# Kernel optimization log

Measured on AMD Instinct MI355X. Metric: run time of the kernel, lower is better.

The kernel has to match this reference:

```python
import jax, jax.numpy as jnp
import numpy as np


def setup_inputs() -> dict:
    key = jax.random.key(0)
    ks = jax.random.split(key, 5)
    B, T, D, H = 32, 2048, 512, 512
    return {
        "x": jax.random.normal(ks[0], (B, T, D), dtype=jnp.float32),
        "W_w": jax.random.normal(ks[1], (4 * H, D), dtype=jnp.float32) * 0.05,
        "W_b": jax.random.normal(ks[2], (4 * H,), dtype=jnp.float32) * 0.05,
        "U_w": jax.random.normal(ks[3], (4 * H, H), dtype=jnp.float32) * 0.05,
        "U_b": jax.random.normal(ks[4], (4 * H,), dtype=jnp.float32) * 0.05,
        "alpha": jnp.ones((H,), dtype=jnp.float32),
    }


def reference(x, W_w, W_b, U_w, U_b, alpha):
    B, T, D = x.shape
    H = alpha.shape[0]
    # Precompute input projection for all timesteps: [B, T, 4H]
    wx = jnp.einsum("btd,gd->btg", x, W_w) + W_b
    h0 = jnp.zeros((B, H), dtype=x.dtype)
    c0 = jnp.zeros((B, H), dtype=x.dtype)

    def step(carry, wx_t):
        h, c = carry
        gates = wx_t + h @ U_w.T + U_b  # [B, 4H]
        i, f, o, g = jnp.split(gates, 4, axis=-1)
        i = jax.nn.sigmoid(i)
        f = jax.nn.sigmoid(f)
        o = jax.nn.sigmoid(o)
        g = jnp.tanh(g)
        c = alpha * (f * c + i * g)
        h = o * jnp.tanh(c)
        return (h, c), h

    (h, c), outs = jax.lax.scan(step, (h0, c0), jnp.swapaxes(wx, 0, 1))
    outs = jnp.swapaxes(outs, 0, 1)  # [B, T, H]
    return outs, (h, c)
```

## Files before the change

kernel.cpp:

```cpp
#include <hip/hip_runtime.h>

#define TT 2048
#define BB 32
#define HH 512
#define NWG 32

typedef _Float16 half8 __attribute__((ext_vector_type(8)));
typedef float f32x4 __attribute__((ext_vector_type(4)));

__device__ __forceinline__ float fsig(float x) { return 1.f / (1.f + __expf(-x)); }
__device__ __forceinline__ float ftanh_(float x) {
  x = fminf(fmaxf(x, -15.f), 15.f);
  float e = __expf(2.f * x);
  return (e - 1.f) / (e + 1.f);
}

__global__ void cvt_f32_f16(const float* __restrict__ in, _Float16* __restrict__ out, int n4) {
  int i = blockIdx.x * 256 + threadIdx.x;
  if (i >= n4) return;
  float4 v = ((const float4*)in)[i];
  union { _Float16 h[4]; unsigned long long u; } r;
  r.h[0] = (_Float16)v.x; r.h[1] = (_Float16)v.y;
  r.h[2] = (_Float16)v.z; r.h[3] = (_Float16)v.w;
  ((unsigned long long*)out)[i] = r.u;
}

__global__ __launch_bounds__(256, 2) void gemm_wx(const _Float16* __restrict__ A,
                                                  const _Float16* __restrict__ Bw,
                                                  _Float16* __restrict__ C) {
  const int bn = blockIdx.x;
  const int bm = blockIdx.y;
  const int tid = threadIdx.x;
  const int lane = tid & 63;
  const int w = tid >> 6;
  __shared__ _Float16 As[128 * 40];
  __shared__ _Float16 Bs[128 * 40];
  const int moff = (w & 1) * 64;
  const int noff = (w >> 1) * 64;
  const int fm = lane & 15;
  const int kq = lane >> 4;
  f32x4 acc[4][4] = {};
  for (int kt = 0; kt < 16; ++kt) {
#pragma unroll
    for (int e = 0; e < 2; ++e) {
      int ci = tid * 2 + e;
      int r = ci >> 2, c16 = ci & 3;
      half8 av = *(const half8*)(A + (size_t)(bm * 128 + r) * 512 + kt * 32 + c16 * 8);
      half8 bv = *(const half8*)(Bw + (size_t)(bn * 128 + r) * 512 + kt * 32 + c16 * 8);
      *(half8*)(As + r * 40 + c16 * 8) = av;
      *(half8*)(Bs + r * 40 + c16 * 8) = bv;
    }
    __syncthreads();
    half8 af[4], bf[4];
#pragma unroll
    for (int i = 0; i < 4; ++i) {
      af[i] = *(const half8*)(As + (moff + i * 16 + fm) * 40 + kq * 8);
      bf[i] = *(const half8*)(Bs + (noff + i * 16 + fm) * 40 + kq * 8);
    }
#pragma unroll
    for (int i = 0; i < 4; ++i)
#pragma unroll
      for (int j = 0; j < 4; ++j)
        acc[i][j] = __builtin_amdgcn_mfma_f32_16x16x32_f16(af[i], bf[j], acc[i][j], 0, 0, 0);
    __syncthreads();
  }
#pragma unroll
  for (int i = 0; i < 4; ++i) {
    int row = bm * 128 + moff + i * 16 + (lane >> 4) * 4;
#pragma unroll
    for (int j = 0; j < 4; ++j) {
      int col = bn * 128 + noff + j * 16 + (lane & 15);
#pragma unroll
      for (int r = 0; r < 4; ++r)
        C[(size_t)(row + r) * 2048 + col] = (_Float16)acc[i][j][r];
    }
  }
}

__global__ __launch_bounds__(256, 1) void slstm_scan(
    const _Float16* __restrict__ wx,
    const _Float16* __restrict__ U16,
    const float* __restrict__ Wb, const float* __restrict__ Ub,
    const float* __restrict__ alpha,
    _Float16* __restrict__ hex,
    int* __restrict__ flags,
    float* __restrict__ out) {
  const int g = blockIdx.x;
  const int tid = threadIdx.x;
  const int lane = tid & 63;
  const int w = tid >> 6;
  const int mi = w & 1;
  const int qA = (w >> 1) * 2;
  const int ncol = lane & 15;
  const int kq = lane >> 4;
  const int am = mi * 16 + ncol;

  half8 Bf0[16], Bf1[16];
#pragma unroll
  for (int ks = 0; ks < 16; ++ks) {
    Bf0[ks] = *(const half8*)(U16 + (size_t)(qA * 512 + g * 16 + ncol) * 512 + ks * 32 + kq * 8);
    Bf1[ks] = *(const half8*)(U16 + (size_t)((qA + 1) * 512 + g * 16 + ncol) * 512 + ks * 32 + kq * 8);
  }

  const int eb = tid >> 3;
  const int jp = tid & 7;
  const int gj0 = g * 16 + jp * 2;
  float bias0[4], bias1[4];
#pragma unroll
  for (int q = 0; q < 4; ++q) {
    bias0[q] = Wb[q * 512 + gj0] + Ub[q * 512 + gj0];
    bias1[q] = Wb[q * 512 + gj0 + 1] + Ub[q * 512 + gj0 + 1];
  }
  const float al0 = alpha[gj0], al1 = alpha[gj0 + 1];
  float c0 = 0.f, c1 = 0.f;

  __shared__ float Sg[4 * 32 * 18];
  __shared__ _Float16 Swx[4 * 32 * 16];

  const int lq = tid >> 6;
  const int lb = (tid >> 1) & 31;
  const int lc = tid & 1;
  const _Float16* wxp = wx + (size_t)lb * TT * 2048 + lq * 512 + g * 16 + lc * 8;

  int spin_budget = 1 << 23;
  const int fl = lane & 31;

  for (int t = 0; t < TT; ++t) {
    half8 wxv = *(const half8*)(wxp + (size_t)t * 2048);
    f32x4 acc0 = {0.f, 0.f, 0.f, 0.f}, acc1 = {0.f, 0.f, 0.f, 0.f};
    if (t > 0) {
      int* fp = flags + (size_t)(t - 1) * 32;
      int v;
      do {
        v = __hip_atomic_load(fp + fl, __ATOMIC_RELAXED, __HIP_MEMORY_SCOPE_AGENT);
        if (--spin_budget <= 0) break;
      } while (!__all(v != 0));
      asm volatile("" ::: "memory");
      unsigned long long* hb64 =
          (unsigned long long*)(hex + ((t & 1) ^ 1) * (BB * HH) + (size_t)am * HH);
      union { unsigned long long u[2]; half8 h; } af[16];
#pragma unroll
      for (int ks = 0; ks < 16; ++ks) {
        af[ks].u[0] = __hip_atomic_load(hb64 + ks * 8 + kq * 2,
                                        __ATOMIC_RELAXED, __HIP_MEMORY_SCOPE_AGENT);
        af[ks].u[1] = __hip_atomic_load(hb64 + ks * 8 + kq * 2 + 1,
                                        __ATOMIC_RELAXED, __HIP_MEMORY_SCOPE_AGENT);
      }
#pragma unroll
      for (int ks = 0; ks < 16; ++ks) {
        acc0 = __builtin_amdgcn_mfma_f32_16x16x32_f16(af[ks].h, Bf0[ks], acc0, 0, 0, 0);
        acc1 = __builtin_amdgcn_mfma_f32_16x16x32_f16(af[ks].h, Bf1[ks], acc1, 0, 0, 0);
      }
    }
    *(half8*)(Swx + (lq * 32 + lb) * 16 + lc * 8) = wxv;
#pragma unroll
    for (int i = 0; i < 4; ++i) {
      int m = mi * 16 + kq * 4 + i;
      Sg[(qA * 32 + m) * 18 + ncol] = acc0[i];
      Sg[((qA + 1) * 32 + m) * 18 + ncol] = acc1[i];
    }
    __syncthreads();
    float p0[4], p1[4];
#pragma unroll
    for (int q = 0; q < 4; ++q) {
      const int so = (q * 32 + eb) * 18 + jp * 2;
      const int wo = (q * 32 + eb) * 16 + jp * 2;
      p0[q] = Sg[so] + (float)Swx[wo] + bias0[q];
      p1[q] = Sg[so + 1] + (float)Swx[wo + 1] + bias1[q];
    }
    float i0 = fsig(p0[0]), f0 = fsig(p0[1]), o0 = fsig(p0[2]), g0 = ftanh_(p0[3]);
    float i1 = fsig(p1[0]), f1 = fsig(p1[1]), o1 = fsig(p1[2]), g1 = ftanh_(p1[3]);
    c0 = al0 * (f0 * c0 + i0 * g0);
    c1 = al1 * (f1 * c1 + i1 * g1);
    float h0 = o0 * ftanh_(c0);
    float h1 = o1 * ftanh_(c1);
    union { _Float16 h[2]; unsigned int u; } pk;
    pk.h[0] = (_Float16)h0; pk.h[1] = (_Float16)h1;
    unsigned int* hx = (unsigned int*)hex + ((t & 1) * (BB * HH) + eb * HH + gj0) / 2;
    __hip_atomic_store(hx, pk.u, __ATOMIC_RELAXED, __HIP_MEMORY_SCOPE_AGENT);
    asm volatile("s_waitcnt vmcnt(0)" ::: "memory");
    __syncthreads();
    if (tid == 0)
      __hip_atomic_store(flags + (size_t)t * 32 + g, 1,
                         __ATOMIC_RELAXED, __HIP_MEMORY_SCOPE_AGENT);
    size_t ob = ((size_t)eb * TT + t) * HH + gj0;
    union { float f[2]; double d; } od;
    od.f[0] = h0; od.f[1] = h1;
    __builtin_nontemporal_store(od.d, (double*)(out + ob));
    if (t == TT - 1) {
      const size_t HB = (size_t)BB * TT * HH;
      out[HB + eb * HH + gj0] = h0;
      out[HB + eb * HH + gj0 + 1] = h1;
      out[HB + BB * HH + eb * HH + gj0] = c0;
      out[HB + BB * HH + eb * HH + gj0 + 1] = c1;
    }
  }
}

extern "C" void kernel_launch(void* const* d_in, const int* in_sizes, int n_in,
                              void* d_out, int out_size, void* d_ws, size_t ws_size,
                              hipStream_t stream) {
  (void)in_sizes; (void)n_in; (void)out_size; (void)ws_size;
  const float* x  = (const float*)d_in[0];
  const float* Ww = (const float*)d_in[1];
  const float* Wb = (const float*)d_in[2];
  const float* Uw = (const float*)d_in[3];
  const float* Ub = (const float*)d_in[4];
  const float* al = (const float*)d_in[5];
  float* out = (float*)d_out;

  char* p = (char*)d_ws;
  _Float16* x16  = (_Float16*)p; p += (size_t)BB * TT * 512 * 2;
  _Float16* wx16 = (_Float16*)p; p += (size_t)BB * TT * 2048 * 2;
  _Float16* U16  = (_Float16*)p; p += (size_t)2048 * 512 * 2;
  _Float16* W16  = (_Float16*)p; p += (size_t)2048 * 512 * 2;
  _Float16* hexb = (_Float16*)p; p += (size_t)2 * BB * HH * 2;
  int* flags     = (int*)p;      p += (size_t)TT * 32 * 4;

  (void)hipMemsetAsync(flags, 0, (size_t)TT * 32 * 4, stream);
  cvt_f32_f16<<<32768, 256, 0, stream>>>(x, x16, BB * TT * 512 / 4);
  cvt_f32_f16<<<1024, 256, 0, stream>>>(Ww, W16, 2048 * 512 / 4);
  cvt_f32_f16<<<1024, 256, 0, stream>>>(Uw, U16, 2048 * 512 / 4);
  gemm_wx<<<dim3(16, 512), 256, 0, stream>>>(x16, W16, wx16);
  slstm_scan<<<NWG, 256, 0, stream>>>(wx16, U16, Wb, Ub, al, hexb, flags, out);
}
```

Baseline: 12.21 ms.

## Replace flag-based inter-block sync with sentinel-filled per-timestep hidden-state buffer

Drops the per-timestep flag array and the write, wait, barrier and flag-store handshake. Each timestep now writes h into its own slice of a buffer pre-filled with 0xFF (a NaN sentinel, reusing the x16 workspace after the GEMM), and consumers spin directly on the h data until no sentinel values remain. This removes one round trip of global-memory latency per step on the serial critical path. In exchange it costs a large memset and relies on no valid fp16 h pair matching the sentinel pattern, and it only checks that each 32-bit word was written, not the ordering of separate stores.

```diff
diff --git a/kernel.cpp b/kernel.cpp
--- a/kernel.cpp
+++ b/kernel.cpp
@@ -83,7 +83,6 @@
     const float* __restrict__ Wb, const float* __restrict__ Ub,
     const float* __restrict__ alpha,
     _Float16* __restrict__ hex,
-    int* __restrict__ flags,
     float* __restrict__ out) {
   const int g = blockIdx.x;
   const int tid = threadIdx.x;
@@ -122,29 +121,33 @@
   const int lc = tid & 1;
   const _Float16* wxp = wx + (size_t)lb * TT * 2048 + lq * 512 + g * 16 + lc * 8;
 
-  int spin_budget = 1 << 23;
-  const int fl = lane & 31;
+  int spin_budget = 1 << 22;
 
   for (int t = 0; t < TT; ++t) {
     half8 wxv = *(const half8*)(wxp + (size_t)t * 2048);
     f32x4 acc0 = {0.f, 0.f, 0.f, 0.f}, acc1 = {0.f, 0.f, 0.f, 0.f};
     if (t > 0) {
-      int* fp = flags + (size_t)(t - 1) * 32;
-      int v;
-      do {
-        v = __hip_atomic_load(fp + fl, __ATOMIC_RELAXED, __HIP_MEMORY_SCOPE_AGENT);
+      const unsigned long long* hb64 =
+          (const unsigned long long*)(hex + (size_t)(t - 1) * (BB * HH) + (size_t)am * HH);
+      union { unsigned long long u[2]; half8 h; } af[16];
+      for (;;) {
+        unsigned mx = 0;
+#pragma unroll
+        for (int ks = 0; ks < 16; ++ks) {
+          af[ks].u[0] = __hip_atomic_load(hb64 + ks * 8 + kq * 2,
+                                          __ATOMIC_RELAXED, __HIP_MEMORY_SCOPE_AGENT);
+          af[ks].u[1] = __hip_atomic_load(hb64 + ks * 8 + kq * 2 + 1,
+                                          __ATOMIC_RELAXED, __HIP_MEMORY_SCOPE_AGENT);
+        }
+#pragma unroll
+        for (int ks = 0; ks < 16; ++ks) {
+          unsigned a = (unsigned)af[ks].u[0], b = (unsigned)(af[ks].u[0] >> 32);
+          unsigned c = (unsigned)af[ks].u[1], d = (unsigned)(af[ks].u[1] >> 32);
+          mx = mx > a ? mx : a; mx = mx > b ? mx : b;
+          mx = mx > c ? mx : c; mx = mx > d ? mx : d;
+        }
+        if (__all(mx < 0xFFFF0000u)) break;
         if (--spin_budget <= 0) break;
-      } while (!__all(v != 0));
-      asm volatile("" ::: "memory");
-      unsigned long long* hb64 =
-          (unsigned long long*)(hex + ((t & 1) ^ 1) * (BB * HH) + (size_t)am * HH);
-      union { unsigned long long u[2]; half8 h; } af[16];
-#pragma unroll
-      for (int ks = 0; ks < 16; ++ks) {
-        af[ks].u[0] = __hip_atomic_load(hb64 + ks * 8 + kq * 2,
-                                        __ATOMIC_RELAXED, __HIP_MEMORY_SCOPE_AGENT);
-        af[ks].u[1] = __hip_atomic_load(hb64 + ks * 8 + kq * 2 + 1,
-                                        __ATOMIC_RELAXED, __HIP_MEMORY_SCOPE_AGENT);
       }
 #pragma unroll
       for (int ks = 0; ks < 16; ++ks) {
@@ -176,13 +179,8 @@
     float h1 = o1 * ftanh_(c1);
     union { _Float16 h[2]; unsigned int u; } pk;
     pk.h[0] = (_Float16)h0; pk.h[1] = (_Float16)h1;
-    unsigned int* hx = (unsigned int*)hex + ((t & 1) * (BB * HH) + eb * HH + gj0) / 2;
+    unsigned int* hx = (unsigned int*)hex + ((size_t)t * (BB * HH) + eb * HH + gj0) / 2;
     __hip_atomic_store(hx, pk.u, __ATOMIC_RELAXED, __HIP_MEMORY_SCOPE_AGENT);
-    asm volatile("s_waitcnt vmcnt(0)" ::: "memory");
-    __syncthreads();
-    if (tid == 0)
-      __hip_atomic_store(flags + (size_t)t * 32 + g, 1,
-                         __ATOMIC_RELAXED, __HIP_MEMORY_SCOPE_AGENT);
     size_t ob = ((size_t)eb * TT + t) * HH + gj0;
     union { float f[2]; double d; } od;
     od.f[0] = h0; od.f[1] = h1;
@@ -194,6 +192,7 @@
       out[HB + BB * HH + eb * HH + gj0] = c0;
       out[HB + BB * HH + eb * HH + gj0 + 1] = c1;
     }
+    __syncthreads();
   }
 }
 
@@ -214,13 +213,12 @@
   _Float16* wx16 = (_Float16*)p; p += (size_t)BB * TT * 2048 * 2;
   _Float16* U16  = (_Float16*)p; p += (size_t)2048 * 512 * 2;
   _Float16* W16  = (_Float16*)p; p += (size_t)2048 * 512 * 2;
-  _Float16* hexb = (_Float16*)p; p += (size_t)2 * BB * HH * 2;
-  int* flags     = (int*)p;      p += (size_t)TT * 32 * 4;
-
-  (void)hipMemsetAsync(flags, 0, (size_t)TT * 32 * 4, stream);
+  _Float16* hexb = x16;
+
   cvt_f32_f16<<<32768, 256, 0, stream>>>(x, x16, BB * TT * 512 / 4);
   cvt_f32_f16<<<1024, 256, 0, stream>>>(Ww, W16, 2048 * 512 / 4);
   cvt_f32_f16<<<1024, 256, 0, stream>>>(Uw, U16, 2048 * 512 / 4);
   gemm_wx<<<dim3(16, 512), 256, 0, stream>>>(x16, W16, wx16);
-  slstm_scan<<<NWG, 256, 0, stream>>>(wx16, U16, Wb, Ub, al, hexb, flags, out);
-}
+  (void)hipMemsetAsync(hexb, 0xFF, (size_t)TT * BB * HH * 2, stream);
+  slstm_scan<<<NWG, 256, 0, stream>>>(wx16, U16, Wb, Ub, al, hexb, out);
+}
```

Measured after the change: 14.73 ms. 1.21x slower.
